# Kernel optimization log

Hardware: AMD Instinct MI355X
Metric: run time of the kernel (lower is better)

## Reference

```python
import jax, jax.numpy as jnp
import numpy as np

V, D, H = 5000, 300, 256
B, T = 16, 512


def setup_inputs() -> dict:
    key = jax.random.key(0)
    ks = jax.random.split(key, 14)
    def w(k, shape):
        return jax.random.normal(k, shape, dtype=jnp.float32) * 0.02
    return {
        "x": jax.random.normal(ks[0], (B, T, V), dtype=jnp.float32),
        "hidden_state": jax.random.normal(ks[1], (1, H), dtype=jnp.float32),
        "context_state": jax.random.normal(ks[2], (1, H), dtype=jnp.float32),
        "E": w(ks[3], (D, V)),      # embedding Linear weight [out,in]
        "Wf": w(ks[4], (H, D)), "Uf": w(ks[5], (H, H)),
        "Wg": w(ks[6], (H, D)), "Ug": w(ks[7], (H, H)),
        "Wi": w(ks[8], (H, D)), "Ui": w(ks[9], (H, H)),
        "Wo": w(ks[10], (H, D)), "Uo": w(ks[11], (H, H)),
        "Wout": w(ks[12], (V, H)),
    }


def reference(x, hidden_state, context_state, E, Wf, Uf, Wg, Ug, Wi, Ui, Wo, Uo, Wout):
    # Precompute all input-side projections in one batched pass: [B,T,D]
    emb = jnp.einsum('btv,dv->btd', x, E)
    # Stack input-gate GEMMs: [B,T,4H]
    Wx = jnp.concatenate([Wf, Wg, Wi, Wo], axis=0)  # [4H, D]
    gates_x = jnp.einsum('btd,gd->btg', emb, Wx)    # [B, T, 4H]
    Uh = jnp.concatenate([Uf, Ug, Ui, Uo], axis=0)  # [4H, H]

    h0 = jnp.broadcast_to(hidden_state, (x.shape[0], hidden_state.shape[-1]))
    c0 = jnp.broadcast_to(context_state, (x.shape[0], context_state.shape[-1]))

    Hn = hidden_state.shape[-1]

    def step(carry, gx):
        h, c = carry
        gh = h @ Uh.T                     # [B, 4H]
        z = gx + gh
        f = jax.nn.sigmoid(z[:, 0*Hn:1*Hn])
        g = jnp.tanh(z[:, 1*Hn:2*Hn])
        i = jax.nn.sigmoid(z[:, 2*Hn:3*Hn])
        o = jax.nn.sigmoid(z[:, 3*Hn:4*Hn])
        c_new = g * i + c * f
        h_new = o * jnp.tanh(c_new)
        # NOTE: faithful to source - output projects g, not h
        out = g @ Wout.T                  # [B, V]
        return (h_new, c_new), out

    _, outs = jax.lax.scan(step, (h0, c0), jnp.swapaxes(gates_x, 0, 1))
    return jnp.swapaxes(outs, 0, 1)       # [B, T, V]
```

## Files before the change

### kernel.cpp

```cpp
#include <hip/hip_runtime.h>
#include <stdint.h>

typedef unsigned short u16;
typedef unsigned int u32;
typedef __attribute__((ext_vector_type(8))) __bf16 bf16x8;
typedef __attribute__((ext_vector_type(4))) float f32x4;
typedef __attribute__((ext_vector_type(4))) u32 u32x4;
typedef __attribute__((ext_vector_type(2))) u32 u32x2;
typedef __attribute__((ext_vector_type(4))) int i32x4;

#define DEV __device__ __forceinline__

constexpr int V = 5000, D = 300, H = 256, BB = 16, T = 512;
constexpr int M = BB * T;
constexpr int DP = 320;
constexpr int KP = 5024;
constexpr int G4 = 1024;
constexpr int NPAD = 5120;

constexpr size_t OFF_EB    = 0;
constexpr size_t OFF_WXB   = OFF_EB    + (size_t)DP * KP * 2;
constexpr size_t OFF_UHB   = OFF_WXB   + (size_t)G4 * DP * 2;
constexpr size_t OFF_WOUTB = OFF_UHB   + (size_t)G4 * H * 2;
constexpr size_t OFF_GATES = OFF_WOUTB + (size_t)NPAD * H * 2;
constexpr size_t OFF_GALL  = OFF_GATES + (size_t)T * BB * G4 * 2;
constexpr size_t OFF_EMB   = OFF_GALL  + (size_t)M * H * 2;

DEV u16 f2bf(float f) {
  u32 i = __builtin_bit_cast(u32, f);
  return (u16)((i + 0x7FFFu + ((i >> 16) & 1u)) >> 16);
}
DEV float bf2f(u16 u) { return __builtin_bit_cast(float, (u32)u << 16); }
DEV f32x4 MFMA(u32x4 a, u32x4 b, f32x4 c) {
  return __builtin_amdgcn_mfma_f32_16x16x32_bf16(
      __builtin_bit_cast(bf16x8, a), __builtin_bit_cast(bf16x8, b), c, 0, 0, 0);
}
DEV i32x4 MFMA8(u32x4 a, u32x4 b, i32x4 c) {
  return __builtin_amdgcn_mfma_i32_16x16x64_i8(
      __builtin_bit_cast(i32x4, a), __builtin_bit_cast(i32x4, b), c, 0, 0, 0);
}
DEV float sigm(float x) { return 1.f / (1.f + __expf(-x)); }
DEV float tanh_s(float x) { float e = __expf(2.f * x); return 1.f - 2.f / (e + 1.f); }

DEV void bar_lds() {
  asm volatile("s_waitcnt lgkmcnt(0)" ::: "memory");
  __builtin_amdgcn_sched_barrier(0);
  __builtin_amdgcn_s_barrier();
  __builtin_amdgcn_sched_barrier(0);
}

__global__ __launch_bounds__(256) void k_prep(
    const float* __restrict__ E, const float* __restrict__ Wf, const float* __restrict__ Wg,
    const float* __restrict__ Wi, const float* __restrict__ Wo,
    const float* __restrict__ Wout, char* __restrict__ ws) {
  u16* Eb = (u16*)(ws + OFF_EB);
  u16* Wxb = (u16*)(ws + OFF_WXB);
  u16* Wob = (u16*)(ws + OFF_WOUTB);

  const int NE = DP * KP, NW = G4 * DP, NWO = NPAD * H;
  const int total = NE + NW + NWO;
  for (int i = blockIdx.x * blockDim.x + threadIdx.x; i < total; i += gridDim.x * blockDim.x) {
    int j = i;
    if (j < NE) {
      int nn = j / KP, k = j % KP;
      Eb[j] = f2bf((nn < D && k < V) ? E[(size_t)nn * V + k] : 0.f);
      continue;
    }
    j -= NE;
    if (j < NW) {
      int r = j / DP, k = j % DP;
      const float* Wp = (r < 256) ? Wf : (r < 512) ? Wg : (r < 768) ? Wi : Wo;
      Wxb[j] = f2bf((k < D) ? Wp[(size_t)(r & 255) * D + k] : 0.f);
      continue;
    }
    j -= NW;
    if (j < NWO) {
      int nn = j / H, k = j % H;
      Wob[j] = f2bf((nn < V) ? Wout[(size_t)nn * H + k] : 0.f);
      continue;
    }
  }
}

__global__ __launch_bounds__(256) void k_prep_u(
    const float* __restrict__ Uf, const float* __restrict__ Ug,
    const float* __restrict__ Ui, const float* __restrict__ Uo, char* __restrict__ ws) {
  char* qU = ws + OFF_UHB;
  float* zsc = (float*)(ws + OFF_UHB + (size_t)G4 * H);
  const int row = blockIdx.x * 4 + (threadIdx.x >> 6);
  const int lane = threadIdx.x & 63;
  const float* Up = (row < 256) ? Uf : (row < 512) ? Ug : (row < 768) ? Ui : Uo;
  f32x4 v = *(const f32x4*)(Up + (size_t)(row & 255) * H + lane * 4);
  float m = fmaxf(fmaxf(fabsf(v[0]), fabsf(v[1])), fmaxf(fabsf(v[2]), fabsf(v[3])));
  for (int i = 1; i < 64; i <<= 1) m = fmaxf(m, __shfl_xor(m, i));
  float inv = (m > 0.f) ? 127.f / m : 0.f;
  int q0 = (int)rintf(v[0] * inv), q1 = (int)rintf(v[1] * inv);
  int q2 = (int)rintf(v[2] * inv), q3 = (int)rintf(v[3] * inv);
  q0 = max(-127, min(127, q0)); q1 = max(-127, min(127, q1));
  q2 = max(-127, min(127, q2)); q3 = max(-127, min(127, q3));
  u32 pk = (u32)(q0 & 255) | ((u32)(q1 & 255) << 8) | ((u32)(q2 & 255) << 16) |
           ((u32)(q3 & 255) << 24);
  *(u32*)(qU + (size_t)row * H + lane * 4) = pk;
  if (lane == 0) zsc[row] = m / 16129.f;
}

__global__ __launch_bounds__(256) void k_emb(const float* __restrict__ x, char* __restrict__ ws) {
  const u16* Eb = (const u16*)(ws + OFF_EB);
  float* emb = (float*)(ws + OFF_EMB);
  __shared__ __align__(16) u16 As[32 * 40];
  __shared__ __align__(16) u16 Bs[320 * 40];

  const int tid = threadIdx.x;
  const int m0 = blockIdx.x * 32;
  const int lane = tid & 63, wv = tid >> 6;
  const int l15 = lane & 15, lc = lane >> 4;
  const int mt = wv & 1, ntb = (wv >> 1) * 10;

  f32x4 acc[10];
#pragma unroll
  for (int j = 0; j < 10; j++) acc[j] = (f32x4){0.f, 0.f, 0.f, 0.f};

  const int ar = tid >> 3, ak = (tid & 7) * 4;

  f32x4 xv0, xv1;
  u32x4 ev0[5], ev1[5];

#define EMB_ISSUE(SFX, KS)                                                        \
  do {                                                                            \
    int k0_ = (KS) * 32;                                                          \
    {                                                                             \
      size_t base_ = (size_t)(m0 + ar) * V + k0_ + ak;                            \
      if (k0_ + ak + 3 < V) {                                                     \
        xv##SFX = *(const f32x4*)(x + base_);                                     \
      } else {                                                                    \
        f32x4 t_;                                                                 \
        t_[0] = (k0_ + ak + 0 < V) ? x[base_ + 0] : 0.f;                          \
        t_[1] = (k0_ + ak + 1 < V) ? x[base_ + 1] : 0.f;                          \
        t_[2] = (k0_ + ak + 2 < V) ? x[base_ + 2] : 0.f;                          \
        t_[3] = (k0_ + ak + 3 < V) ? x[base_ + 3] : 0.f;                          \
        xv##SFX = t_;                                                             \
      }                                                                           \
    }                                                                             \
    _Pragma("unroll") for (int j_ = 0; j_ < 5; j_++) {                            \
      int cc_ = tid + 256 * j_;                                                   \
      int n_ = cc_ >> 2, ko_ = (cc_ & 3) * 8;                                     \
      ev##SFX[j_] = *(const u32x4*)(Eb + (size_t)n_ * KP + k0_ + ko_);            \
    }                                                                             \
  } while (0)

#define EMB_WRITE(SFX)                                                            \
  do {                                                                            \
    union { u16 u[4]; u32x2 v; } ua_;                                             \
    ua_.u[0] = f2bf(xv##SFX[0]); ua_.u[1] = f2bf(xv##SFX[1]);                     \
    ua_.u[2] = f2bf(xv##SFX[2]); ua_.u[3] = f2bf(xv##SFX[3]);                     \
    *(u32x2*)&As[ar * 40 + ak] = ua_.v;                                           \
    _Pragma("unroll") for (int j_ = 0; j_ < 5; j_++) {                            \
      int cc_ = tid + 256 * j_;                                                   \
      int n_ = cc_ >> 2, ko_ = (cc_ & 3) * 8;                                     \
      *(u32x4*)&Bs[n_ * 40 + ko_] = ev##SFX[j_];                                  \
    }                                                                             \
  } while (0)

  auto emb_compute = [&]() {
    u32x4 a = *(const u32x4*)&As[(mt * 16 + l15) * 40 + lc * 8];
#pragma unroll
    for (int j = 0; j < 10; j++) {
      u32x4 b = *(const u32x4*)&Bs[((ntb + j) * 16 + l15) * 40 + lc * 8];
      acc[j] = MFMA(a, b, acc[j]);
    }
  };

  constexpr int NK = 157;
  EMB_ISSUE(0, 0);
  EMB_ISSUE(1, 1);
  for (int ks = 0; ks < NK; ks += 2) {
    __syncthreads();
    EMB_WRITE(0);
    if (ks + 2 < NK) EMB_ISSUE(0, ks + 2);
    __syncthreads();
    emb_compute();
    if (ks + 1 < NK) {
      __syncthreads();
      EMB_WRITE(1);
      if (ks + 3 < NK) EMB_ISSUE(1, ks + 3);
      __syncthreads();
      emb_compute();
    }
  }
#pragma unroll
  for (int j = 0; j < 10; j++) {
    int nn = (ntb + j) * 16 + l15;
    int mrow = m0 + mt * 16 + lc * 4;
#pragma unroll
    for (int r = 0; r < 4; r++) emb[(size_t)(mrow + r) * DP + nn] = acc[j][r];
  }
#undef EMB_ISSUE
#undef EMB_WRITE
}

__global__ __launch_bounds__(256) void k_gates(char* __restrict__ ws) {
  const float* emb = (const float*)(ws + OFF_EMB);
  const u16* Wxb = (const u16*)(ws + OFF_WXB);
  u16* gates = (u16*)(ws + OFF_GATES);
  __shared__ __align__(16) u16 As[64 * 40];
  __shared__ __align__(16) u16 Bs[256 * 40];

  const int tid = threadIdx.x;
  const int blk = blockIdx.x;
  const int m0 = (blk >> 2) * 64, n0 = (blk & 3) * 256;
  const int lane = tid & 63, wv = tid >> 6;
  const int l15 = lane & 15, lc = lane >> 4;

  f32x4 acc[16];
#pragma unroll
  for (int j = 0; j < 16; j++) acc[j] = (f32x4){0.f, 0.f, 0.f, 0.f};

  f32x4 av0[2], av1[2];
  u32x4 bv0[4], bv1[4];

#define GT_ISSUE(SFX, KS)                                                         \
  do {                                                                            \
    int k0_ = (KS) * 32;                                                          \
    _Pragma("unroll") for (int j_ = 0; j_ < 2; j_++) {                            \
      int c_ = tid + 256 * j_;                                                    \
      int r_ = c_ >> 3, ko_ = (c_ & 7) * 4;                                       \
      av##SFX[j_] = *(const f32x4*)(emb + (size_t)(m0 + r_) * DP + k0_ + ko_);    \
    }                                                                             \
    _Pragma("unroll") for (int j_ = 0; j_ < 4; j_++) {                            \
      int c_ = tid + 256 * j_;                                                    \
      int n_ = c_ >> 2, ko_ = (c_ & 3) * 8;                                       \
      bv##SFX[j_] = *(const u32x4*)(Wxb + (size_t)(n0 + n_) * DP + k0_ + ko_);    \
    }                                                                             \
  } while (0)

#define GT_WRITE(SFX)                                                             \
  do {                                                                            \
    _Pragma("unroll") for (int j_ = 0; j_ < 2; j_++) {                            \
      int c_ = tid + 256 * j_;                                                    \
      int r_ = c_ >> 3, ko_ = (c_ & 7) * 4;                                       \
      union { u16 u[4]; u32x2 v; } ua_;                                           \
      ua_.u[0] = f2bf(av##SFX[j_][0]); ua_.u[1] = f2bf(av##SFX[j_][1]);           \
      ua_.u[2] = f2bf(av##SFX[j_][2]); ua_.u[3] = f2bf(av##SFX[j_][3]);           \
      *(u32x2*)&As[r_ * 40 + ko_] = ua_.v;                                        \
    }                                                                             \
    _Pragma("unroll") for (int j_ = 0; j_ < 4; j_++) {                            \
      int c_ = tid + 256 * j_;                                                    \
      int n_ = c_ >> 2, ko_ = (c_ & 3) * 8;                                       \
      *(u32x4*)&Bs[n_ * 40 + ko_] = bv##SFX[j_];                                  \
    }                                                                             \
  } while (0)

  auto gt_compute = [&]() {
    u32x4 a = *(const u32x4*)&As[(wv * 16 + l15) * 40 + lc * 8];
#pragma unroll
    for (int nt = 0; nt < 16; nt++) {
      u32x4 b = *(const u32x4*)&Bs[(nt * 16 + l15) * 40 + lc * 8];
      acc[nt] = MFMA(a, b, acc[nt]);
    }
  };

  constexpr int NK = 10;
  GT_ISSUE(0, 0);
  GT_ISSUE(1, 1);
  for (int ks = 0; ks < NK; ks += 2) {
    __syncthreads();
    GT_WRITE(0);
    if (ks + 2 < NK) GT_ISSUE(0, ks + 2);
    __syncthreads();
    gt_compute();
    __syncthreads();
    GT_WRITE(1);
    if (ks + 3 < NK) GT_ISSUE(1, ks + 3);
    __syncthreads();
    gt_compute();
  }
#pragma unroll
  for (int nt = 0; nt < 16; nt++) {
#pragma unroll
    for (int r = 0; r < 4; r++) {
      int m = m0 + wv * 16 + lc * 4 + r;
      int col = n0 + nt * 16 + l15;
      int q = col >> 8, nn = col & 255;
      gates[(((size_t)(m & (T - 1)) * 16 + (m >> 9)) * 256 + nn) * 4 + q] = f2bf(acc[nt][r]);
    }
  }
#undef GT_ISSUE
#undef GT_WRITE
}

__global__ __launch_bounds__(512) void k_scan(const float* __restrict__ hidden,
                                              const float* __restrict__ ctx,
                                              char* __restrict__ ws) {
  const char* qU = (const char*)(ws + OFF_UHB);
  const float* zsc = (const float*)(ws + OFF_UHB + (size_t)G4 * H);
  const u16* gates = (const u16*)(ws + OFF_GATES);
  u16* gall = (u16*)(ws + OFF_GALL);

  __shared__ __align__(16) char pq[2][2][256];
  __shared__ __align__(16) int zw[2][8][8][2][16];

  const int tid = threadIdx.x;
  const int lane = tid & 63, wv = tid >> 6;
  const int l15 = lane & 15, lc = lane >> 4;

  u32x4 uq[4][2][4];
#pragma unroll
  for (int gg = 0; gg < 4; gg++)
#pragma unroll
    for (int j = 0; j < 2; j++)
#pragma unroll
      for (int kt = 0; kt < 4; kt++)
        uq[gg][j][kt] = *(const u32x4*)(
            qU + (size_t)(gg * 256 + wv * 32 + j * 16 + l15) * H + kt * 64 + lc * 16);

  const int b = lane >> 5, np = lane & 31;
  const int n = wv * 32 + np;
  const int jj = (np >> 4) & 1, rr = np & 15;
  const int b_glob = blockIdx.x * 2 + b;
  float c = ctx[n];
  const float zs0 = zsc[n], zs1 = zsc[n + 256], zs2 = zsc[n + 512], zs3 = zsc[n + 768];
  u32x2 gxc = *(const u32x2*)(gates + (((size_t)0 * 16 + b_glob) * 256 + n) * 4);
  u32x2 gxn = *(const u32x2*)(gates + (((size_t)1 * 16 + b_glob) * 256 + n) * 4);

  {
    const int b0 = tid >> 8, n0i = tid & 255;
    float h0 = hidden[n0i];
    h0 = fminf(3.999f, fmaxf(-3.999f, h0));
    pq[0][b0][n0i] = (char)(int)rintf(h0 * 31.75f);
  }
  __syncthreads();

#pragma unroll 1
  for (int t = 0; t < T; ++t) {
    const int par = t & 1;
    u32x4 bfr[4];
#pragma unroll
    for (int kt = 0; kt < 4; kt++)
      bfr[kt] = *(const u32x4*)&pq[par][l15 & 1][kt * 64 + lc * 16];

    i32x4 acc[4][2];
#pragma unroll
    for (int gg = 0; gg < 4; gg++)
#pragma unroll
      for (int j = 0; j < 2; j++) {
        i32x4 a = {0, 0, 0, 0};
#pragma unroll
        for (int kt = 0; kt < 4; kt++) a = MFMA8(uq[gg][j][kt], bfr[kt], a);
        acc[gg][j] = a;
      }
    if (l15 < 2) {
#pragma unroll
      for (int gg = 0; gg < 4; gg++)
#pragma unroll
        for (int j = 0; j < 2; j++)
          *(i32x4*)&zw[par][wv][gg * 2 + j][l15][lc * 4] = acc[gg][j];
    }
    asm volatile("s_waitcnt lgkmcnt(0)" ::: "memory");
    __builtin_amdgcn_sched_barrier(0);

    const float hs = (t == 0) ? 4.f : 1.f;
    float z0 = (float)zw[par][wv][0 + jj][b][rr] * (zs0 * hs) + bf2f((u16)(gxc[0] & 0xFFFFu));
    float z1 = (float)zw[par][wv][2 + jj][b][rr] * (zs1 * hs) + bf2f((u16)(gxc[0] >> 16));
    float z2 = (float)zw[par][wv][4 + jj][b][rr] * (zs2 * hs) + bf2f((u16)(gxc[1] & 0xFFFFu));
    float z3 = (float)zw[par][wv][6 + jj][b][rr] * (zs3 * hs) + bf2f((u16)(gxc[1] >> 16));
    float fv = sigm(z0), gv = tanh_s(z1), iv = sigm(z2), ov = sigm(z3);
    c = gv * iv + c * fv;
    float hn = ov * tanh_s(c);
    gall[((size_t)b_glob * T + t) * H + n] = f2bf(gv);
    pq[par ^ 1][b][n] = (char)(int)rintf(hn * 127.f);
    gxc = gxn;
    int t2 = (t + 2 < T) ? (t + 2) : t;
    gxn = *(const u32x2*)(gates + (((size_t)t2 * 16 + b_glob) * 256 + n) * 4);
    bar_lds();
  }
}

__global__ __launch_bounds__(256) void k_out(char* __restrict__ ws, float* __restrict__ out) {
  const u16* gall = (const u16*)(ws + OFF_GALL);
  const u16* Wob = (const u16*)(ws + OFF_WOUTB);
  __shared__ __align__(16) u16 As[64 * 40];
  __shared__ __align__(16) u16 Bs[256 * 40];

  const int tid = threadIdx.x;
  const int blk = blockIdx.x;
  const int m0 = (blk / 20) * 64, n0 = (blk % 20) * 256;
  const int lane = tid & 63, wv = tid >> 6;
  const int l15 = lane & 15, lc = lane >> 4;

  f32x4 acc[16];
#pragma unroll
  for (int j = 0; j < 16; j++) acc[j] = (f32x4){0.f, 0.f, 0.f, 0.f};

  u32x4 av0, av1;
  u32x4 bv0[4], bv1[4];

#define OUT_ISSUE(SFX, KS)                                                        \
  do {                                                                            \
    int k0_ = (KS) * 32;                                                          \
    {                                                                             \
      int r_ = tid >> 2, ko_ = (tid & 3) * 8;                                     \
      av##SFX = *(const u32x4*)(gall + (size_t)(m0 + r_) * H + k0_ + ko_);        \
    }                                                                             \
    _Pragma("unroll") for (int j_ = 0; j_ < 4; j_++) {                            \
      int c_ = tid + 256 * j_;                                                    \
      int n_ = c_ >> 2, ko_ = (c_ & 3) * 8;                                       \
      bv##SFX[j_] = *(const u32x4*)(Wob + (size_t)(n0 + n_) * H + k0_ + ko_);     \
    }                                                                             \
  } while (0)

#define OUT_WRITE(SFX)                                                            \
  do {                                                                            \
    {                                                                             \
      int r_ = tid >> 2, ko_ = (tid & 3) * 8;                                     \
      *(u32x4*)&As[r_ * 40 + ko_] = av##SFX;                                      \
    }                                                                             \
    _Pragma("unroll") for (int j_ = 0; j_ < 4; j_++) {                            \
      int c_ = tid + 256 * j_;                                                    \
      int n_ = c_ >> 2, ko_ = (c_ & 3) * 8;                                       \
      *(u32x4*)&Bs[n_ * 40 + ko_] = bv##SFX[j_];                                  \
    }                                                                             \
  } while (0)

  auto out_compute = [&]() {
    u32x4 a = *(const u32x4*)&As[(wv * 16 + l15) * 40 + lc * 8];
#pragma unroll
    for (int nt = 0; nt < 16; nt++) {
      u32x4 b = *(const u32x4*)&Bs[(nt * 16 + l15) * 40 + lc * 8];
      acc[nt] = MFMA(a, b, acc[nt]);
    }
  };

  constexpr int NK = 8;
  OUT_ISSUE(0, 0);
  OUT_ISSUE(1, 1);
  for (int ks = 0; ks < NK; ks += 2) {
    __syncthreads();
    OUT_WRITE(0);
    if (ks + 2 < NK) OUT_ISSUE(0, ks + 2);
    __syncthreads();
    out_compute();
    __syncthreads();
    OUT_WRITE(1);
    if (ks + 3 < NK) OUT_ISSUE(1, ks + 3);
    __syncthreads();
    out_compute();
  }
#pragma unroll
  for (int nt = 0; nt < 16; nt++) {
    int vcol = n0 + nt * 16 + l15;
    if (vcol < V) {
#pragma unroll
      for (int r = 0; r < 4; r++) {
        int m = m0 + wv * 16 + lc * 4 + r;
        out[(size_t)m * V + vcol] = acc[nt][r];
      }
    }
  }
#undef OUT_ISSUE
#undef OUT_WRITE
}

extern "C" void kernel_launch(void* const* d_in, const int* in_sizes, int n_in,
                              void* d_out, int out_size, void* d_ws, size_t ws_size,
                              hipStream_t stream) {
  (void)in_sizes; (void)n_in; (void)out_size; (void)ws_size;
  const float* x      = (const float*)d_in[0];
  const float* hidden = (const float*)d_in[1];
  const float* ctx    = (const float*)d_in[2];
  const float* E      = (const float*)d_in[3];
  const float* Wf     = (const float*)d_in[4];
  const float* Uf     = (const float*)d_in[5];
  const float* Wg     = (const float*)d_in[6];
  const float* Ug     = (const float*)d_in[7];
  const float* Wi     = (const float*)d_in[8];
  const float* Ui     = (const float*)d_in[9];
  const float* Wo     = (const float*)d_in[10];
  const float* Uo     = (const float*)d_in[11];
  const float* Wout   = (const float*)d_in[12];
  char* ws = (char*)d_ws;
  float* out = (float*)d_out;

  hipLaunchKernelGGL(k_prep, dim3(1024), dim3(256), 0, stream,
                     E, Wf, Wg, Wi, Wo, Wout, ws);
  hipLaunchKernelGGL(k_prep_u, dim3(256), dim3(256), 0, stream, Uf, Ug, Ui, Uo, ws);
  hipLaunchKernelGGL(k_emb, dim3(M / 32), dim3(256), 0, stream, x, ws);
  hipLaunchKernelGGL(k_gates, dim3((M / 64) * 4), dim3(256), 0, stream, ws);
  hipLaunchKernelGGL(k_scan, dim3(8), dim3(512), 0, stream, hidden, ctx, ws);
  hipLaunchKernelGGL(k_out, dim3((M / 64) * 20), dim3(256), 0, stream, ws, out);
}
```

Before: 822.8 us.

## Fuse emb, gates, scan and output GEMMs into one persistent kernel with flag sync

Result: slower. 936.3 us (+13.8%).

```diff
diff --git a/kernel.cpp b/kernel.cpp
--- a/kernel.cpp
+++ b/kernel.cpp
@@ -17,6 +17,8 @@
 constexpr int KP = 5024;
 constexpr int G4 = 1024;
 constexpr int NPAD = 5120;
+constexpr int NWRK = 128;
+constexpr int EMBS_ST = 328;
 
 constexpr size_t OFF_EB    = 0;
 constexpr size_t OFF_WXB   = OFF_EB    + (size_t)DP * KP * 2;
@@ -24,7 +26,7 @@
 constexpr size_t OFF_WOUTB = OFF_UHB   + (size_t)G4 * H * 2;
 constexpr size_t OFF_GATES = OFF_WOUTB + (size_t)NPAD * H * 2;
 constexpr size_t OFF_GALL  = OFF_GATES + (size_t)T * BB * G4 * 2;
-constexpr size_t OFF_EMB   = OFF_GALL  + (size_t)M * H * 2;
+constexpr size_t OFF_SYNC  = OFF_GALL  + (size_t)M * H * 2;
 
 DEV u16 f2bf(float f) {
   u32 i = __builtin_bit_cast(u32, f);
@@ -47,6 +49,20 @@
   __builtin_amdgcn_sched_barrier(0);
   __builtin_amdgcn_s_barrier();
   __builtin_amdgcn_sched_barrier(0);
+}
+DEV u32 ld32_cohere(const u32* p) {
+  u32 v;
+  asm volatile("global_load_dword %0, %1, off sc0 sc1\n\ts_waitcnt vmcnt(0)"
+               : "=v"(v) : "v"(p) : "memory");
+  return v;
+}
+DEV void st32_cohere(u32* p, u32 v) {
+  asm volatile("global_store_dword %0, %1, off sc0 sc1" :: "v"(p), "v"(v) : "memory");
+}
+DEV u32x4 ld16_cohere(const void* p) {
+  u32x4 v;
+  asm volatile("global_load_dwordx4 %0, %1, off sc0 sc1" : "=v"(v) : "v"(p));
+  return v;
 }
 
 __global__ __launch_bounds__(256) void k_prep(
@@ -58,7 +74,7 @@
   u16* Wob = (u16*)(ws + OFF_WOUTB);
 
   const int NE = DP * KP, NW = G4 * DP, NWO = NPAD * H;
-  const int total = NE + NW + NWO;
+  const int total = NE + NW + NWO + 32;
   for (int i = blockIdx.x * blockDim.x + threadIdx.x; i < total; i += gridDim.x * blockDim.x) {
     int j = i;
     if (j < NE) {
@@ -79,6 +95,8 @@
       Wob[j] = f2bf((nn < V) ? Wout[(size_t)nn * H + k] : 0.f);
       continue;
     }
+    j -= NWO;
+    if (j < 32) ((u32*)(ws + OFF_SYNC))[j] = 0u;
   }
 }
 
@@ -104,32 +122,142 @@
   if (lane == 0) zsc[row] = m / 16129.f;
 }
 
-__global__ __launch_bounds__(256) void k_emb(const float* __restrict__ x, char* __restrict__ ws) {
-  const u16* Eb = (const u16*)(ws + OFF_EB);
-  float* emb = (float*)(ws + OFF_EMB);
-  __shared__ __align__(16) u16 As[32 * 40];
-  __shared__ __align__(16) u16 Bs[320 * 40];
-
+__global__ __launch_bounds__(512) void k_fused(const float* __restrict__ x,
+                                               const float* __restrict__ hidden,
+                                               const float* __restrict__ ctx,
+                                               char* __restrict__ ws,
+                                               float* __restrict__ out) {
+  __shared__ __align__(16) char smem[49152];
   const int tid = threadIdx.x;
-  const int m0 = blockIdx.x * 32;
   const int lane = tid & 63, wv = tid >> 6;
   const int l15 = lane & 15, lc = lane >> 4;
-  const int mt = wv & 1, ntb = (wv >> 1) * 10;
-
-  f32x4 acc[10];
-#pragma unroll
-  for (int j = 0; j < 10; j++) acc[j] = (f32x4){0.f, 0.f, 0.f, 0.f};
-
-  const int ar = tid >> 3, ak = (tid & 7) * 4;
-
-  f32x4 xv0, xv1;
-  u32x4 ev0[5], ev1[5];
-
-#define EMB_ISSUE(SFX, KS)                                                        \
+  u32* flag = (u32*)(ws + OFF_SYNC);
+  u32* prog = (u32*)(ws + OFF_SYNC + 64);
+
+  if (blockIdx.x < 8) {
+    __builtin_amdgcn_s_setprio(1);
+    const char* qU = (const char*)(ws + OFF_UHB);
+    const float* zsc = (const float*)(ws + OFF_UHB + (size_t)G4 * H);
+    const u16* gates = (const u16*)(ws + OFF_GATES);
+    u16* gall = (u16*)(ws + OFF_GALL);
+    char* pqp = smem;
+    int* zwp = (int*)(smem + 1024);
+
+    const int g = blockIdx.x;
+    u32x4 uq[4][2][4];
+#pragma unroll
+    for (int gg = 0; gg < 4; gg++)
+#pragma unroll
+      for (int j = 0; j < 2; j++)
+#pragma unroll
+        for (int kt = 0; kt < 4; kt++)
+          uq[gg][j][kt] = *(const u32x4*)(
+              qU + (size_t)(gg * 256 + wv * 32 + j * 16 + l15) * H + kt * 64 + lc * 16);
+
+    const int b = lane >> 5, np = lane & 31;
+    const int n = wv * 32 + np;
+    const int jj = (np >> 4) & 1, rr = np & 15;
+    const int b_glob = g * 2 + b;
+    float c = ctx[n];
+    const float zs0 = zsc[n], zs1 = zsc[n + 256], zs2 = zsc[n + 512], zs3 = zsc[n + 768];
+
+    {
+      const int b0 = tid >> 8, n0i = tid & 255;
+      float h0 = hidden[n0i];
+      h0 = fminf(3.999f, fmaxf(-3.999f, h0));
+      pqp[(0 * 2 + b0) * 256 + n0i] = (char)(int)rintf(h0 * 31.75f);
+    }
+    if (tid == 0) {
+      while (ld32_cohere(&flag[0]) < 16u) __builtin_amdgcn_s_sleep(8);
+    }
+    __syncthreads();
+
+    u32x2 gxc = *(const u32x2*)(gates + (((size_t)0 * 16 + b_glob) * 256 + n) * 4);
+    u32x2 gxn = *(const u32x2*)(gates + (((size_t)1 * 16 + b_glob) * 256 + n) * 4);
+
+#pragma unroll 1
+    for (int t = 0; t < T; ++t) {
+      const int par = t & 1;
+      if (((t + 2) & 31) == 0 && (t + 2) < T) {
+        const int ck = (t + 2) >> 5;
+        if (tid == 0) {
+          while (ld32_cohere(&flag[ck]) < 16u) __builtin_amdgcn_s_sleep(8);
+        }
+        bar_lds();
+      }
+      u32x4 bfr[4];
+#pragma unroll
+      for (int kt = 0; kt < 4; kt++)
+        bfr[kt] = *(const u32x4*)&pqp[(par * 2 + (l15 & 1)) * 256 + kt * 64 + lc * 16];
+
+      i32x4 acc[4][2];
+#pragma unroll
+      for (int gg = 0; gg < 4; gg++)
+#pragma unroll
+        for (int j = 0; j < 2; j++) {
+          i32x4 a = {0, 0, 0, 0};
+#pragma unroll
+          for (int kt = 0; kt < 4; kt++) a = MFMA8(uq[gg][j][kt], bfr[kt], a);
+          acc[gg][j] = a;
+        }
+      if (l15 < 2) {
+#pragma unroll
+        for (int gg = 0; gg < 4; gg++)
+#pragma unroll
+          for (int j = 0; j < 2; j++)
+            *(i32x4*)&zwp[(((par * 8 + wv) * 8 + gg * 2 + j) * 2 + l15) * 16 + lc * 4] =
+                acc[gg][j];
+      }
+      asm volatile("s_waitcnt lgkmcnt(0)" ::: "memory");
+      __builtin_amdgcn_sched_barrier(0);
+
+      const float hs = (t == 0) ? 4.f : 1.f;
+      float z0 = (float)zwp[(((par * 8 + wv) * 8 + 0 + jj) * 2 + b) * 16 + rr] * (zs0 * hs) +
+                 bf2f((u16)(gxc[0] & 0xFFFFu));
+      float z1 = (float)zwp[(((par * 8 + wv) * 8 + 2 + jj) * 2 + b) * 16 + rr] * (zs1 * hs) +
+                 bf2f((u16)(gxc[0] >> 16));
+      float z2 = (float)zwp[(((par * 8 + wv) * 8 + 4 + jj) * 2 + b) * 16 + rr] * (zs2 * hs) +
+                 bf2f((u16)(gxc[1] & 0xFFFFu));
+      float z3 = (float)zwp[(((par * 8 + wv) * 8 + 6 + jj) * 2 + b) * 16 + rr] * (zs3 * hs) +
+                 bf2f((u16)(gxc[1] >> 16));
+      float fv = sigm(z0), gv = tanh_s(z1), iv = sigm(z2), ov = sigm(z3);
+      c = gv * iv + c * fv;
+      float hn = ov * tanh_s(c);
+      gall[((size_t)b_glob * T + t) * H + n] = f2bf(gv);
+      pqp[((par ^ 1) * 2 + b) * 256 + n] = (char)(int)rintf(hn * 127.f);
+      gxc = gxn;
+      int t2 = (t + 2 < T) ? (t + 2) : t;
+      gxn = *(const u32x2*)(gates + (((size_t)t2 * 16 + b_glob) * 256 + n) * 4);
+      if ((t & 31) == 31) __threadfence();
+      bar_lds();
+      if ((t & 31) == 31 && tid == 0) st32_cohere(&prog[g], (u32)(t + 1));
+    }
+  } else {
+    const int wid = blockIdx.x - 8;
+    u16* As = (u16*)smem;
+    u16* Bs = (u16*)(smem + 2560);
+    u16* embS = (u16*)(smem + 28160);
+    const u16* Eb = (const u16*)(ws + OFF_EB);
+    const u16* Wxb = (const u16*)(ws + OFF_WXB);
+    u16* gates = (u16*)(ws + OFF_GATES);
+    const u16* gall = (const u16*)(ws + OFF_GALL);
+    const u16* Wob = (const u16*)(ws + OFF_WOUTB);
+
+    for (int it = wid; it < 256; it += NWRK) {
+      const int tc = it >> 4, b = it & 15;
+      const int m0x = b * T + tc * 32;
+      f32x4 acc[5];
+#pragma unroll
+      for (int j = 0; j < 5; j++) acc[j] = (f32x4){0.f, 0.f, 0.f, 0.f};
+      const int ar = tid >> 3, ak = (tid & 7) * 4;
+      f32x4 xv0, xv1;
+      u32x4 ev0[3], ev1[3];
+
+#define WEMB_ISSUE(SFX, KS)                                                       \
   do {                                                                            \
     int k0_ = (KS) * 32;                                                          \
-    {                                                                             \
-      size_t base_ = (size_t)(m0 + ar) * V + k0_ + ak;                            \
+    if (tid < 256) {                                                              \
+      size_t base_ = (size_t)(m0x + ar) * V + k0_ + ak;                           \
       if (k0_ + ak + 3 < V) {                                                     \
         xv##SFX = *(const f32x4*)(x + base_);                                     \
       } else {                                                                    \
@@ -141,323 +269,138 @@
         xv##SFX = t_;                                                             \
       }                                                                           \
     }                                                                             \
-    _Pragma("unroll") for (int j_ = 0; j_ < 5; j_++) {                            \
-      int cc_ = tid + 256 * j_;                                                   \
-      int n_ = cc_ >> 2, ko_ = (cc_ & 3) * 8;                                     \
-      ev##SFX[j_] = *(const u32x4*)(Eb + (size_t)n_ * KP + k0_ + ko_);            \
+    _Pragma("unroll") for (int p_ = 0; p_ < 3; p_++) {                            \
+      int cc_ = tid + 512 * p_;                                                   \
+      if (cc_ < 1280) {                                                           \
+        int n_ = cc_ >> 2, ko_ = (cc_ & 3) * 8;                                   \
+        ev##SFX[p_] = *(const u32x4*)(Eb + (size_t)n_ * KP + k0_ + ko_);          \
+      }                                                                           \
     }                                                                             \
   } while (0)
 
-#define EMB_WRITE(SFX)                                                            \
+#define WEMB_WRITE(SFX)                                                           \
   do {                                                                            \
-    union { u16 u[4]; u32x2 v; } ua_;                                             \
-    ua_.u[0] = f2bf(xv##SFX[0]); ua_.u[1] = f2bf(xv##SFX[1]);                     \
-    ua_.u[2] = f2bf(xv##SFX[2]); ua_.u[3] = f2bf(xv##SFX[3]);                     \
-    *(u32x2*)&As[ar * 40 + ak] = ua_.v;                                           \
-    _Pragma("unroll") for (int j_ = 0; j_ < 5; j_++) {                            \
-      int cc_ = tid + 256 * j_;                                                   \
-      int n_ = cc_ >> 2, ko_ = (cc_ & 3) * 8;                                     \
-      *(u32x4*)&Bs[n_ * 40 + ko_] = ev##SFX[j_];                                  \
+    if (tid < 256) {                                                              \
+      union { u16 u[4]; u32x2 v; } ua_;                                           \
+      ua_.u[0] = f2bf(xv##SFX[0]); ua_.u[1] = f2bf(xv##SFX[1]);                   \
+      ua_.u[2] = f2bf(xv##SFX[2]); ua_.u[3] = f2bf(xv##SFX[3]);                   \
+      *(u32x2*)&As[ar * 40 + ak] = ua_.v;                                         \
+    }                                                                             \
+    _Pragma("unroll") for (int p_ = 0; p_ < 3; p_++) {                            \
+      int cc_ = tid + 512 * p_;                                                   \
+      if (cc_ < 1280) {                                                           \
+        int n_ = cc_ >> 2, ko_ = (cc_ & 3) * 8;                                   \
+        *(u32x4*)&Bs[n_ * 40 + ko_] = ev##SFX[p_];                                \
+      }                                                                           \
     }                                                                             \
   } while (0)
 
-  auto emb_compute = [&]() {
-    u32x4 a = *(const u32x4*)&As[(mt * 16 + l15) * 40 + lc * 8];
-#pragma unroll
-    for (int j = 0; j < 10; j++) {
-      u32x4 b = *(const u32x4*)&Bs[((ntb + j) * 16 + l15) * 40 + lc * 8];
-      acc[j] = MFMA(a, b, acc[j]);
-    }
-  };
-
-  constexpr int NK = 157;
-  EMB_ISSUE(0, 0);
-  EMB_ISSUE(1, 1);
-  for (int ks = 0; ks < NK; ks += 2) {
-    __syncthreads();
-    EMB_WRITE(0);
-    if (ks + 2 < NK) EMB_ISSUE(0, ks + 2);
-    __syncthreads();
-    emb_compute();
-    if (ks + 1 < NK) {
+      const int mt = wv & 1, ntb = (wv >> 1) * 5;
+      auto wemb_compute = [&]() {
+        u32x4 a = *(const u32x4*)&As[(mt * 16 + l15) * 40 + lc * 8];
+#pragma unroll
+        for (int j = 0; j < 5; j++) {
+          u32x4 bb = *(const u32x4*)&Bs[((ntb + j) * 16 + l15) * 40 + lc * 8];
+          acc[j] = MFMA(a, bb, acc[j]);
+        }
+      };
+
+      constexpr int NK = 157;
+      WEMB_ISSUE(0, 0);
+      WEMB_ISSUE(1, 1);
+      for (int ks = 0; ks < NK; ks += 2) {
+        __syncthreads();
+        WEMB_WRITE(0);
+        if (ks + 2 < NK) WEMB_ISSUE(0, ks + 2);
+        __syncthreads();
+        wemb_compute();
+        if (ks + 1 < NK) {
+          __syncthreads();
+          WEMB_WRITE(1);
+          if (ks + 3 < NK) WEMB_ISSUE(1, ks + 3);
+          __syncthreads();
+          wemb_compute();
+        }
+      }
+#undef WEMB_ISSUE
+#undef WEMB_WRITE
       __syncthreads();
-      EMB_WRITE(1);
-      if (ks + 3 < NK) EMB_ISSUE(1, ks + 3);
+#pragma unroll
+      for (int j = 0; j < 5; j++) {
+        int nn = (ntb + j) * 16 + l15;
+#pragma unroll
+        for (int r = 0; r < 4; r++)
+          embS[(mt * 16 + lc * 4 + r) * EMBS_ST + nn] = f2bf(acc[j][r]);
+      }
       __syncthreads();
-      emb_compute();
+
+      const int amt = wv & 1, ngrp = wv >> 1;
+      f32x4 gacc[16];
+#pragma unroll
+      for (int j = 0; j < 16; j++) gacc[j] = (f32x4){0.f, 0.f, 0.f, 0.f};
+#pragma unroll 1
+      for (int kc = 0; kc < 10; kc++) {
+        u32x4 a = *(const u32x4*)&embS[(amt * 16 + l15) * EMBS_ST + kc * 32 + lc * 8];
+#pragma unroll
+        for (int nt = 0; nt < 16; nt++) {
+          int col = ngrp * 256 + nt * 16 + l15;
+          u32x4 bb = *(const u32x4*)(Wxb + (size_t)col * DP + kc * 32 + lc * 8);
+          gacc[nt] = MFMA(a, bb, gacc[nt]);
+        }
+      }
+#pragma unroll
+      for (int nt = 0; nt < 16; nt++) {
+#pragma unroll
+        for (int r = 0; r < 4; r++) {
+          int t = tc * 32 + amt * 16 + lc * 4 + r;
+          int col = ngrp * 256 + nt * 16 + l15;
+          int q = col >> 8, nn = col & 255;
+          gates[(((size_t)t * 16 + b) * 256 + nn) * 4 + q] = f2bf(gacc[nt][r]);
+        }
+      }
+      __threadfence();
+      __syncthreads();
+      if (tid == 0) atomicAdd(&flag[tc], 1u);
+    }
+
+    for (int it = wid; it < 2560; it += NWRK) {
+      const int tk = it / 320, rem = it % 320;
+      const int b = rem / 20, nb = rem % 20;
+      const int g = b >> 1;
+      const u32 need = (u32)((tk + 1) * 64);
+      if (tid == 0) {
+        while (ld32_cohere(&prog[g]) < need) __builtin_amdgcn_s_sleep(8);
+      }
+      __syncthreads();
+
+      const int amt = wv & 3, nh = wv >> 2;
+      const int m0 = b * T + tk * 64, n0 = nb * 256 + nh * 128;
+      f32x4 acc[8];
+#pragma unroll
+      for (int j = 0; j < 8; j++) acc[j] = (f32x4){0.f, 0.f, 0.f, 0.f};
+#pragma unroll 1
+      for (int ks = 0; ks < 8; ks++) {
+        u32x4 a = ld16_cohere((const char*)gall +
+                              2 * ((size_t)(m0 + amt * 16 + l15) * H + ks * 32 + lc * 8));
+#pragma unroll
+        for (int nt = 0; nt < 8; nt++) {
+          u32x4 bb = *(const u32x4*)(Wob + (size_t)(n0 + nt * 16 + l15) * H + ks * 32 + lc * 8);
+          acc[nt] = MFMA(a, bb, acc[nt]);
+        }
+      }
+#pragma unroll
+      for (int nt = 0; nt < 8; nt++) {
+        int vcol = n0 + nt * 16 + l15;
+        if (vcol < V) {
+#pragma unroll
+          for (int r = 0; r < 4; r++) {
+            int m = m0 + amt * 16 + lc * 4 + r;
+            out[(size_t)m * V + vcol] = acc[nt][r];
+          }
+        }
+      }
     }
   }
-#pragma unroll
-  for (int j = 0; j < 10; j++) {
-    int nn = (ntb + j) * 16 + l15;
-    int mrow = m0 + mt * 16 + lc * 4;
-#pragma unroll
-    for (int r = 0; r < 4; r++) emb[(size_t)(mrow + r) * DP + nn] = acc[j][r];
-  }
-#undef EMB_ISSUE
-#undef EMB_WRITE
-}
-
-__global__ __launch_bounds__(256) void k_gates(char* __restrict__ ws) {
-  const float* emb = (const float*)(ws + OFF_EMB);
-  const u16* Wxb = (const u16*)(ws + OFF_WXB);
-  u16* gates = (u16*)(ws + OFF_GATES);
-  __shared__ __align__(16) u16 As[64 * 40];
-  __shared__ __align__(16) u16 Bs[256 * 40];
-
-  const int tid = threadIdx.x;
-  const int blk = blockIdx.x;
-  const int m0 = (blk >> 2) * 64, n0 = (blk & 3) * 256;
-  const int lane = tid & 63, wv = tid >> 6;
-  const int l15 = lane & 15, lc = lane >> 4;
-
-  f32x4 acc[16];
-#pragma unroll
-  for (int j = 0; j < 16; j++) acc[j] = (f32x4){0.f, 0.f, 0.f, 0.f};
-
-  f32x4 av0[2], av1[2];
-  u32x4 bv0[4], bv1[4];
-
-#define GT_ISSUE(SFX, KS)                                                         \
-  do {                                                                            \
-    int k0_ = (KS) * 32;                                                          \
-    _Pragma("unroll") for (int j_ = 0; j_ < 2; j_++) {                            \
-      int c_ = tid + 256 * j_;                                                    \
-      int r_ = c_ >> 3, ko_ = (c_ & 7) * 4;                                       \
-      av##SFX[j_] = *(const f32x4*)(emb + (size_t)(m0 + r_) * DP + k0_ + ko_);    \
-    }                                                                             \
-    _Pragma("unroll") for (int j_ = 0; j_ < 4; j_++) {                            \
-      int c_ = tid + 256 * j_;                                                    \
-      int n_ = c_ >> 2, ko_ = (c_ & 3) * 8;                                       \
-      bv##SFX[j_] = *(const u32x4*)(Wxb + (size_t)(n0 + n_) * DP + k0_ + ko_);    \
-    }                                                                             \
-  } while (0)
-
-#define GT_WRITE(SFX)                                                             \
-  do {                                                                            \
-    _Pragma("unroll") for (int j_ = 0; j_ < 2; j_++) {                            \
-      int c_ = tid + 256 * j_;                                                    \
-      int r_ = c_ >> 3, ko_ = (c_ & 7) * 4;                                       \
-      union { u16 u[4]; u32x2 v; } ua_;                                           \
-      ua_.u[0] = f2bf(av##SFX[j_][0]); ua_.u[1] = f2bf(av##SFX[j_][1]);           \
-      ua_.u[2] = f2bf(av##SFX[j_][2]); ua_.u[3] = f2bf(av##SFX[j_][3]);           \
-      *(u32x2*)&As[r_ * 40 + ko_] = ua_.v;                                        \
-    }                                                                             \
-    _Pragma("unroll") for (int j_ = 0; j_ < 4; j_++) {                            \
-      int c_ = tid + 256 * j_;                                                    \
-      int n_ = c_ >> 2, ko_ = (c_ & 3) * 8;                                       \
-      *(u32x4*)&Bs[n_ * 40 + ko_] = bv##SFX[j_];                                  \
-    }                                                                             \
-  } while (0)
-
-  auto gt_compute = [&]() {
-    u32x4 a = *(const u32x4*)&As[(wv * 16 + l15) * 40 + lc * 8];
-#pragma unroll
-    for (int nt = 0; nt < 16; nt++) {
-      u32x4 b = *(const u32x4*)&Bs[(nt * 16 + l15) * 40 + lc * 8];
-      acc[nt] = MFMA(a, b, acc[nt]);
-    }
-  };
-
-  constexpr int NK = 10;
-  GT_ISSUE(0, 0);
-  GT_ISSUE(1, 1);
-  for (int ks = 0; ks < NK; ks += 2) {
-    __syncthreads();
-    GT_WRITE(0);
-    if (ks + 2 < NK) GT_ISSUE(0, ks + 2);
-    __syncthreads();
-    gt_compute();
-    __syncthreads();
-    GT_WRITE(1);
-    if (ks + 3 < NK) GT_ISSUE(1, ks + 3);
-    __syncthreads();
-    gt_compute();
-  }
-#pragma unroll
-  for (int nt = 0; nt < 16; nt++) {
-#pragma unroll
-    for (int r = 0; r < 4; r++) {
-      int m = m0 + wv * 16 + lc * 4 + r;
-      int col = n0 + nt * 16 + l15;
-      int q = col >> 8, nn = col & 255;
-      gates[(((size_t)(m & (T - 1)) * 16 + (m >> 9)) * 256 + nn) * 4 + q] = f2bf(acc[nt][r]);
-    }
-  }
-#undef GT_ISSUE
-#undef GT_WRITE
-}
-
-__global__ __launch_bounds__(512) void k_scan(const float* __restrict__ hidden,
-                                              const float* __restrict__ ctx,
-                                              char* __restrict__ ws) {
-  const char* qU = (const char*)(ws + OFF_UHB);
-  const float* zsc = (const float*)(ws + OFF_UHB + (size_t)G4 * H);
-  const u16* gates = (const u16*)(ws + OFF_GATES);
-  u16* gall = (u16*)(ws + OFF_GALL);
-
-  __shared__ __align__(16) char pq[2][2][256];
-  __shared__ __align__(16) int zw[2][8][8][2][16];
-
-  const int tid = threadIdx.x;
-  const int lane = tid & 63, wv = tid >> 6;
-  const int l15 = lane & 15, lc = lane >> 4;
-
-  u32x4 uq[4][2][4];
-#pragma unroll
-  for (int gg = 0; gg < 4; gg++)
-#pragma unroll
-    for (int j = 0; j < 2; j++)
-#pragma unroll
-      for (int kt = 0; kt < 4; kt++)
-        uq[gg][j][kt] = *(const u32x4*)(
-            qU + (size_t)(gg * 256 + wv * 32 + j * 16 + l15) * H + kt * 64 + lc * 16);
-
-  const int b = lane >> 5, np = lane & 31;
-  const int n = wv * 32 + np;
-  const int jj = (np >> 4) & 1, rr = np & 15;
-  const int b_glob = blockIdx.x * 2 + b;
-  float c = ctx[n];
-  const float zs0 = zsc[n], zs1 = zsc[n + 256], zs2 = zsc[n + 512], zs3 = zsc[n + 768];
-  u32x2 gxc = *(const u32x2*)(gates + (((size_t)0 * 16 + b_glob) * 256 + n) * 4);
-  u32x2 gxn = *(const u32x2*)(gates + (((size_t)1 * 16 + b_glob) * 256 + n) * 4);
-
-  {
-    const int b0 = tid >> 8, n0i = tid & 255;
-    float h0 = hidden[n0i];
-    h0 = fminf(3.999f, fmaxf(-3.999f, h0));
-    pq[0][b0][n0i] = (char)(int)rintf(h0 * 31.75f);
-  }
-  __syncthreads();
-
-#pragma unroll 1
-  for (int t = 0; t < T; ++t) {
-    const int par = t & 1;
-    u32x4 bfr[4];
-#pragma unroll
-    for (int kt = 0; kt < 4; kt++)
-      bfr[kt] = *(const u32x4*)&pq[par][l15 & 1][kt * 64 + lc * 16];
-
-    i32x4 acc[4][2];
-#pragma unroll
-    for (int gg = 0; gg < 4; gg++)
-#pragma unroll
-      for (int j = 0; j < 2; j++) {
-        i32x4 a = {0, 0, 0, 0};
-#pragma unroll
-        for (int kt = 0; kt < 4; kt++) a = MFMA8(uq[gg][j][kt], bfr[kt], a);
-        acc[gg][j] = a;
-      }
-    if (l15 < 2) {
-#pragma unroll
-      for (int gg = 0; gg < 4; gg++)
-#pragma unroll
-        for (int j = 0; j < 2; j++)
-          *(i32x4*)&zw[par][wv][gg * 2 + j][l15][lc * 4] = acc[gg][j];
-    }
-    asm volatile("s_waitcnt lgkmcnt(0)" ::: "memory");
-    __builtin_amdgcn_sched_barrier(0);
-
-    const float hs = (t == 0) ? 4.f : 1.f;
-    float z0 = (float)zw[par][wv][0 + jj][b][rr] * (zs0 * hs) + bf2f((u16)(gxc[0] & 0xFFFFu));
-    float z1 = (float)zw[par][wv][2 + jj][b][rr] * (zs1 * hs) + bf2f((u16)(gxc[0] >> 16));
-    float z2 = (float)zw[par][wv][4 + jj][b][rr] * (zs2 * hs) + bf2f((u16)(gxc[1] & 0xFFFFu));
-    float z3 = (float)zw[par][wv][6 + jj][b][rr] * (zs3 * hs) + bf2f((u16)(gxc[1] >> 16));
-    float fv = sigm(z0), gv = tanh_s(z1), iv = sigm(z2), ov = sigm(z3);
-    c = gv * iv + c * fv;
-    float hn = ov * tanh_s(c);
-    gall[((size_t)b_glob * T + t) * H + n] = f2bf(gv);
-    pq[par ^ 1][b][n] = (char)(int)rintf(hn * 127.f);
-    gxc = gxn;
-    int t2 = (t + 2 < T) ? (t + 2) : t;
-    gxn = *(const u32x2*)(gates + (((size_t)t2 * 16 + b_glob) * 256 + n) * 4);
-    bar_lds();
-  }
-}
-
-__global__ __launch_bounds__(256) void k_out(char* __restrict__ ws, float* __restrict__ out) {
-  const u16* gall = (const u16*)(ws + OFF_GALL);
-  const u16* Wob = (const u16*)(ws + OFF_WOUTB);
-  __shared__ __align__(16) u16 As[64 * 40];
-  __shared__ __align__(16) u16 Bs[256 * 40];
-
-  const int tid = threadIdx.x;
-  const int blk = blockIdx.x;
-  const int m0 = (blk / 20) * 64, n0 = (blk % 20) * 256;
-  const int lane = tid & 63, wv = tid >> 6;
-  const int l15 = lane & 15, lc = lane >> 4;
-
-  f32x4 acc[16];
-#pragma unroll
-  for (int j = 0; j < 16; j++) acc[j] = (f32x4){0.f, 0.f, 0.f, 0.f};
-
-  u32x4 av0, av1;
-  u32x4 bv0[4], bv1[4];
-
-#define OUT_ISSUE(SFX, KS)                                                        \
-  do {                                                                            \
-    int k0_ = (KS) * 32;                                                          \
-    {                                                                             \
-      int r_ = tid >> 2, ko_ = (tid & 3) * 8;                                     \
-      av##SFX = *(const u32x4*)(gall + (size_t)(m0 + r_) * H + k0_ + ko_);        \
-    }                                                                             \
-    _Pragma("unroll") for (int j_ = 0; j_ < 4; j_++) {                            \
-      int c_ = tid + 256 * j_;                                                    \
-      int n_ = c_ >> 2, ko_ = (c_ & 3) * 8;                                       \
-      bv##SFX[j_] = *(const u32x4*)(Wob + (size_t)(n0 + n_) * H + k0_ + ko_);     \
-    }                                                                             \
-  } while (0)
-
-#define OUT_WRITE(SFX)                                                            \
-  do {                                                                            \
-    {                                                                             \
-      int r_ = tid >> 2, ko_ = (tid & 3) * 8;                                     \
-      *(u32x4*)&As[r_ * 40 + ko_] = av##SFX;                                      \
-    }                                                                             \
-    _Pragma("unroll") for (int j_ = 0; j_ < 4; j_++) {                            \
-      int c_ = tid + 256 * j_;                                                    \
-      int n_ = c_ >> 2, ko_ = (c_ & 3) * 8;                                       \
-      *(u32x4*)&Bs[n_ * 40 + ko_] = bv##SFX[j_];                                  \
-    }                                                                             \
-  } while (0)
-
-  auto out_compute = [&]() {
-    u32x4 a = *(const u32x4*)&As[(wv * 16 + l15) * 40 + lc * 8];
-#pragma unroll
-    for (int nt = 0; nt < 16; nt++) {
-      u32x4 b = *(const u32x4*)&Bs[(nt * 16 + l15) * 40 + lc * 8];
-      acc[nt] = MFMA(a, b, acc[nt]);
-    }
-  };
-
-  constexpr int NK = 8;
-  OUT_ISSUE(0, 0);
-  OUT_ISSUE(1, 1);
-  for (int ks = 0; ks < NK; ks += 2) {
-    __syncthreads();
-    OUT_WRITE(0);
-    if (ks + 2 < NK) OUT_ISSUE(0, ks + 2);
-    __syncthreads();
-    out_compute();
-    __syncthreads();
-    OUT_WRITE(1);
-    if (ks + 3 < NK) OUT_ISSUE(1, ks + 3);
-    __syncthreads();
-    out_compute();
-  }
-#pragma unroll
-  for (int nt = 0; nt < 16; nt++) {
-    int vcol = n0 + nt * 16 + l15;
-    if (vcol < V) {
-#pragma unroll
-      for (int r = 0; r < 4; r++) {
-        int m = m0 + wv * 16 + lc * 4 + r;
-        out[(size_t)m * V + vcol] = acc[nt][r];
-      }
-    }
-  }
-#undef OUT_ISSUE
-#undef OUT_WRITE
 }
 
 extern "C" void kernel_launch(void* const* d_in, const int* in_sizes, int n_in,
@@ -483,8 +426,6 @@
   hipLaunchKernelGGL(k_prep, dim3(1024), dim3(256), 0, stream,
                      E, Wf, Wg, Wi, Wo, Wout, ws);
   hipLaunchKernelGGL(k_prep_u, dim3(256), dim3(256), 0, stream, Uf, Ug, Ui, Uo, ws);
-  hipLaunchKernelGGL(k_emb, dim3(M / 32), dim3(256), 0, stream, x, ws);
-  hipLaunchKernelGGL(k_gates, dim3((M / 64) * 4), dim3(256), 0, stream, ws);
-  hipLaunchKernelGGL(k_scan, dim3(8), dim3(512), 0, stream, hidden, ctx, ws);
-  hipLaunchKernelGGL(k_out, dim3((M / 64) * 20), dim3(256), 0, stream, ws, out);
-}
+  hipLaunchKernelGGL(k_fused, dim3(8 + NWRK), dim3(512), 0, stream,
+                     x, hidden, ctx, ws, out);
+}
```
